# Optimization experiments

Measured on AMD Instinct MI355X. Metric: run time of the kernel, lower is better.

The kernel has to match this reference:

```python
import jax, jax.numpy as jnp
import numpy as np

NUM_HEADS = 16

def setup_inputs() -> dict:
    key = jax.random.key(0)
    ks = jax.random.split(key, 9)
    B, S, H = 2, 2048, 1024
    sc = 0.02
    return {
        "x":  jax.random.normal(ks[0], (B, S, H), jnp.float32),
        "Wq": jax.random.normal(ks[1], (H, H), jnp.float32) * sc,
        "bq": jnp.zeros((H,), jnp.float32),
        "Wk": jax.random.normal(ks[2], (H, H), jnp.float32) * sc,
        "bk": jnp.zeros((H,), jnp.float32),
        "Wv": jax.random.normal(ks[3], (H, H), jnp.float32) * sc,
        "bv": jnp.zeros((H,), jnp.float32),
        "Wo": jax.random.normal(ks[4], (H, H), jnp.float32) * sc,
        "bo": jnp.zeros((H,), jnp.float32),
    }

def _split_heads(t, nh):
    B, S, H = t.shape
    return t.reshape(B, S, nh, H // nh).transpose(0, 2, 1, 3)  # [B, nh, S, hd]

def reference(x, Wq, bq, Wk, bk, Wv, bv, Wo, bo):
    # mask_type == 'gaussian', dropout = 0 (eval), return_weights = False
    B, S, H = x.shape
    nh = NUM_HEADS
    q = _split_heads(x @ Wq + bq, nh)  # [B, nh, S, hd]
    k = _split_heads(x @ Wk + bk, nh)
    v = _split_heads(x @ Wv + bv, nh)
    dif = q - k  # elementwise, as in the original
    # exp(-dif @ dif^T / 2)
    score = jnp.exp(-0.5 * jnp.einsum('bhqd,bhkd->bhqk', dif, dif))
    # gaussian mask: 1 strictly above the diagonal, 0 on/below (faithful to source)
    mask = jnp.triu(jnp.ones((S, S), x.dtype), k=1)
    prob = score * mask  # [B, nh, S, S]
    ctx = jnp.einsum('bhqk,bhkd->bhqd', prob, v)  # [B, nh, S, hd]
    ctx = ctx.transpose(0, 2, 1, 3).reshape(B, S, H)
    return ctx @ Wo + bo
```

## Files before the change

kernel.cpp:

```cpp
#include <hip/hip_runtime.h>
#include <math.h>

constexpr int SEQ  = 2048;
constexpr int HID  = 1024;
constexpr int MTOT = 4096;
constexpr int BH   = 32;

typedef _Float16 f16;
typedef _Float16 f16x8 __attribute__((ext_vector_type(8)));
typedef float    f32x4 __attribute__((ext_vector_type(4)));

__device__ __forceinline__ void gld16(const f16* g, f16* l) {
    __builtin_amdgcn_global_load_lds(
        (__attribute__((address_space(1))) void*)g,
        (__attribute__((address_space(3))) void*)l, 16, 0, 0);
}

__global__ __launch_bounds__(256) void prep(const float* __restrict__ x,
                                            const float* __restrict__ Wq,
                                            const float* __restrict__ Wk,
                                            const float* __restrict__ Wv,
                                            const float* __restrict__ Wo,
                                            f16* __restrict__ xh,
                                            f16* __restrict__ WqkT,
                                            f16* __restrict__ WvT,
                                            f16* __restrict__ WoT) {
    __shared__ f16 T[64][72];
    const int z = blockIdx.z;
    const int t = threadIdx.x;

    if (z == 3) {
        const int chunk = blockIdx.y * 16 + blockIdx.x;
        const float* src = x + (size_t)chunk * 16384;
        f16* dst = xh + (size_t)chunk * 16384;
#pragma unroll
        for (int it = 0; it < 16; it++) {
            const int i = it * 1024 + t * 4;
            float4 v = *(const float4*)(src + i);
            f16 o[4] = {(f16)v.x, (f16)v.y, (f16)v.z, (f16)v.w};
            *(ushort4*)(dst + i) = *(ushort4*)o;
        }
        return;
    }

    const float* W  = (z == 0) ? Wq : (z == 1) ? Wv : Wo;
    f16* WT = (z == 0) ? WqkT : (z == 1) ? WvT : WoT;
    const int k0 = blockIdx.x * 64, n0 = blockIdx.y * 64;
    const int r  = t >> 4;
    const int c4 = (t & 15) * 4;
#pragma unroll
    for (int rr = 0; rr < 64; rr += 16) {
        float4 w = *(const float4*)(W + (size_t)(k0 + rr + r) * HID + n0 + c4);
        if (z == 0) {
            float4 w2 = *(const float4*)(Wk + (size_t)(k0 + rr + r) * HID + n0 + c4);
            w.x -= w2.x; w.y -= w2.y; w.z -= w2.z; w.w -= w2.w;
        }
        T[c4 + 0][rr + r] = (f16)w.x;
        T[c4 + 1][rr + r] = (f16)w.y;
        T[c4 + 2][rr + r] = (f16)w.z;
        T[c4 + 3][rr + r] = (f16)w.w;
    }
    __syncthreads();
#pragma unroll
    for (int pp = 0; pp < 2; pp++) {
        const int nr = pp * 32 + (t >> 3);
        const int kc = (t & 7) * 8;
        *(uint4*)(WT + (size_t)(n0 + nr) * HID + k0 + kc) = *(uint4*)(&T[nr][kc]);
    }
}

__global__ __launch_bounds__(256, 4) void proj_gemm(const f16* __restrict__ A,
                                                    const f16* __restrict__ WqkT,
                                                    const f16* __restrict__ WvT,
                                                    const float* __restrict__ bq,
                                                    const float* __restrict__ bk,
                                                    const float* __restrict__ bv,
                                                    f16* __restrict__ dif,
                                                    f16* __restrict__ vT) {
    __shared__ f16 As[128 * 72];
    __shared__ f16 Bs[64 * 64];
    const int t = threadIdx.x;
    const int m0  = blockIdx.x * 128;
    const int n0g = blockIdx.y * 64;
    const bool isv = (n0g >= HID);
    const f16* BT = isv ? WvT : WqkT;
    const int n0 = n0g & (HID - 1);
    const int w = t >> 6, l = t & 63, quad = l >> 4, ln = l & 15;
    const int wm = w * 32;
    const int xk = ln & 7;

    const int srow8 = l >> 3;
    const int soct  = (l & 7) ^ srow8;
    const f16* pa = A  + (size_t)(m0 + w * 32 + srow8) * HID + soct * 8;
    const f16* pb = BT + (size_t)(n0 + w * 16 + srow8) * HID + soct * 8;

    f32x4 acc[2][4] = {};

    for (int k0 = 0; k0 < HID; k0 += 64) {
        __syncthreads();
#pragma unroll
        for (int c = 0; c < 4; c++)
            gld16(pa + (size_t)c * 8 * HID + k0, As + (w * 4 + c) * 512);
#pragma unroll
        for (int c = 0; c < 2; c++)
            gld16(pb + (size_t)c * 8 * HID + k0, Bs + (w * 2 + c) * 512);
        __syncthreads();

#pragma unroll
        for (int kh = 0; kh < 2; kh++) {
            f16x8 af[2], bf[4];
#pragma unroll
            for (int mt = 0; mt < 2; mt++) {
                const int row = wm + mt * 16 + ln;
                const int oct = (kh * 4 + quad) ^ xk;
                af[mt] = *(const f16x8*)(As + row * 64 + oct * 8);
            }
#pragma unroll
            for (int nt = 0; nt < 4; nt++) {
                const int row = nt * 16 + ln;
                const int oct = (kh * 4 + quad) ^ xk;
                bf[nt] = *(const f16x8*)(Bs + row * 64 + oct * 8);
            }
#pragma unroll
            for (int mt = 0; mt < 2; mt++)
#pragma unroll
                for (int nt = 0; nt < 4; nt++)
                    acc[mt][nt] = __builtin_amdgcn_mfma_f32_16x16x32_f16(
                        af[mt], bf[nt], acc[mt][nt], 0, 0, 0);
        }
    }

    __syncthreads();
    const int b_  = m0 >> 11;
    const int s0g = m0 & 2047;
    const int h_  = n0 >> 6;

    if (!isv) {
        float bb[4];
#pragma unroll
        for (int nt = 0; nt < 4; nt++) {
            const int nl = n0 + nt * 16 + ln;
            bb[nt] = bq[nl] - bk[nl];
        }
#pragma unroll
        for (int mt = 0; mt < 2; mt++)
#pragma unroll
            for (int nt = 0; nt < 4; nt++)
#pragma unroll
                for (int r = 0; r < 4; r++) {
                    const int sl = wm + mt * 16 + quad * 4 + r;
                    As[sl * 72 + nt * 16 + ln] = (f16)(acc[mt][nt][r] + bb[nt]);
                }
        __syncthreads();
        f16* base = dif + ((size_t)(b_ * 16 + h_) * SEQ + s0g) * 64;
        const int sl = t >> 1, eo = (t & 1) * 32;
#pragma unroll
        for (int i = 0; i < 4; i++)
            *(uint4*)(base + (size_t)sl * 64 + eo + i * 8) =
                *(uint4*)(&As[sl * 72 + eo + i * 8]);
    } else {
        float bb[4];
#pragma unroll
        for (int nt = 0; nt < 4; nt++)
            bb[nt] = bv[n0 + nt * 16 + ln];
#pragma unroll
        for (int mt = 0; mt < 2; mt++)
#pragma unroll
            for (int nt = 0; nt < 4; nt++)
#pragma unroll
                for (int r = 0; r < 4; r++) {
                    const int sl = wm + mt * 16 + quad * 4 + r;
                    As[(nt * 16 + ln) * 136 + sl] = (f16)(acc[mt][nt][r] + bb[nt]);
                }
        __syncthreads();
        const int eb = t >> 2, so = (t & 3) * 32;
        f16* base = vT + ((size_t)(b_ * 16 + h_) * 64 + eb) * SEQ + s0g + so;
#pragma unroll
        for (int i = 0; i < 4; i++)
            *(uint4*)(base + i * 8) = *(uint4*)(&As[eb * 136 + so + i * 8]);
    }
}

__global__ __launch_bounds__(256) void out_gemm(const f16* __restrict__ C0,
                                                const f16* __restrict__ C1,
                                                const f16* __restrict__ WoT,
                                                const float* __restrict__ bo,
                                                float* __restrict__ out) {
    __shared__ f16 As[2][128 * 72];
    __shared__ f16 Bs[2][64 * 72];
    const int t = threadIdx.x;
    const int m0 = blockIdx.x * 128, n0 = blockIdx.y * 64;
    const int w = t >> 6, l = t & 63, quad = l >> 4, ln = l & 15;
    const int wm = (w >> 1) * 64, wn = (w & 1) * 32;
    const int arow = t >> 1, ahalf = (t & 1) * 32;
    const int brow = t >> 2, boff = (t & 3) * 16;

    const f16* pa0 = C0  + (size_t)(m0 + arow) * HID + ahalf;
    const f16* pa1 = C1  + (size_t)(m0 + arow) * HID + ahalf;
    const f16* pb  = WoT + (size_t)(n0 + brow) * HID + boff;

    f16x8 a0 = *(const f16x8*)(pa0)      + *(const f16x8*)(pa1);
    f16x8 a1 = *(const f16x8*)(pa0 + 8)  + *(const f16x8*)(pa1 + 8);
    f16x8 a2 = *(const f16x8*)(pa0 + 16) + *(const f16x8*)(pa1 + 16);
    f16x8 a3 = *(const f16x8*)(pa0 + 24) + *(const f16x8*)(pa1 + 24);
    uint4 b0 = *(const uint4*)(pb), b1 = *(const uint4*)(pb + 8);

    f32x4 acc[4][2] = {};
    int buf = 0;

    for (int k0 = 0; k0 < HID; k0 += 64) {
        f16* da = As[buf] + arow * 72 + ahalf;
        *(f16x8*)(da)      = a0; *(f16x8*)(da + 8)  = a1;
        *(f16x8*)(da + 16) = a2; *(f16x8*)(da + 24) = a3;
        f16* db = Bs[buf] + brow * 72 + boff;
        *(uint4*)(db) = b0; *(uint4*)(db + 8) = b1;
        __syncthreads();
        if (k0 + 64 < HID) {
            const int kn = k0 + 64;
            a0 = *(const f16x8*)(pa0 + kn)      + *(const f16x8*)(pa1 + kn);
            a1 = *(const f16x8*)(pa0 + kn + 8)  + *(const f16x8*)(pa1 + kn + 8);
            a2 = *(const f16x8*)(pa0 + kn + 16) + *(const f16x8*)(pa1 + kn + 16);
            a3 = *(const f16x8*)(pa0 + kn + 24) + *(const f16x8*)(pa1 + kn + 24);
            b0 = *(const uint4*)(pb + kn); b1 = *(const uint4*)(pb + kn + 8);
        }
#pragma unroll
        for (int kh = 0; kh < 2; kh++) {
            f16x8 af[4], bf[2];
#pragma unroll
            for (int mt = 0; mt < 4; mt++)
                af[mt] = *(const f16x8*)(As[buf] + (wm + mt * 16 + ln) * 72 + kh * 32 + quad * 8);
#pragma unroll
            for (int nt = 0; nt < 2; nt++)
                bf[nt] = *(const f16x8*)(Bs[buf] + (wn + nt * 16 + ln) * 72 + kh * 32 + quad * 8);
#pragma unroll
            for (int mt = 0; mt < 4; mt++)
#pragma unroll
                for (int nt = 0; nt < 2; nt++)
                    acc[mt][nt] = __builtin_amdgcn_mfma_f32_16x16x32_f16(
                        af[mt], bf[nt], acc[mt][nt], 0, 0, 0);
        }
        buf ^= 1;
    }

#pragma unroll
    for (int mt = 0; mt < 4; mt++)
#pragma unroll
        for (int nt = 0; nt < 2; nt++) {
            const int n = n0 + wn + nt * 16 + ln;
            const float bb = bo[n];
            const int m_base = m0 + wm + mt * 16 + quad * 4;
#pragma unroll
            for (int r = 0; r < 4; r++)
                out[(size_t)(m_base + r) * HID + n] =
                    acc[mt][nt][r] * 65536.0f + bb;
        }
}

__global__ __launch_bounds__(256) void attn_f16(const f16* __restrict__ dif,
                                                const f16* __restrict__ vT,
                                                f16* __restrict__ ctx0,
                                                f16* __restrict__ ctx1) {
    __shared__ f16 Qs[64 * 72];
    __shared__ f16 Ks[64 * 72];
    __shared__ f16 Vs[64 * 72];
    __shared__ f16 Ps[64 * 72];

    const int pq = blockIdx.x, bh = blockIdx.y, ks = blockIdx.z;
    f16* Cout = ks ? ctx1 : ctx0;
    const f16* D  = dif + (size_t)bh * SEQ * 64;
    const f16* VT = vT  + (size_t)bh * 64 * SEQ;
    const int b = bh >> 4, h = bh & 15;
    const int t = threadIdx.x, w = t >> 6, l = t & 63, quad = l >> 4, ln = l & 15;
    const int ve = t >> 2, vc = (t & 3) * 16;

    for (int half = 0; half < 2; half++) {
        const int qt = half ? (31 - pq) : pq;
        const int i0 = qt * 64;
        __syncthreads();

#pragma unroll
        for (int rr = 0; rr < 2; rr++) {
            const int o = rr * 2048 + t * 8;
            uint4 v = *(const uint4*)(D + i0 * 64 + o);
            *(uint4*)(Qs + (o >> 6) * 72 + (o & 63)) = v;
        }
        __syncthreads();
        f16x8 aq[2];
#pragma unroll
        for (int kh = 0; kh < 2; kh++)
            aq[kh] = *(const f16x8*)(Qs + (w * 16 + ln) * 72 + kh * 32 + quad * 8);

        f32x4 acc[4] = {};
        const int kt0 = qt + ks;

        uint4 kr0, kr1, vr0, vr1;
        if (kt0 < 32) {
            const int j0 = kt0 * 64;
            kr0 = *(const uint4*)(D + j0 * 64 + t * 8);
            kr1 = *(const uint4*)(D + j0 * 64 + 2048 + t * 8);
            vr0 = *(const uint4*)(VT + (size_t)ve * SEQ + j0 + vc);
            vr1 = *(const uint4*)(VT + (size_t)ve * SEQ + j0 + vc + 8);
        }

        for (int kt = kt0; kt < 32; kt += 2) {
            __syncthreads();

            {
                const int o0 = t * 8, o1 = 2048 + t * 8;
                *(uint4*)(Ks + (o0 >> 6) * 72 + (o0 & 63)) = kr0;
                *(uint4*)(Ks + (o1 >> 6) * 72 + (o1 & 63)) = kr1;
                *(uint4*)(Vs + ve * 72 + vc)     = vr0;
                *(uint4*)(Vs + ve * 72 + vc + 8) = vr1;
            }
            __syncthreads();

            if (kt + 2 < 32) {
                const int j2 = (kt + 2) * 64;
                kr0 = *(const uint4*)(D + j2 * 64 + t * 8);
                kr1 = *(const uint4*)(D + j2 * 64 + 2048 + t * 8);
                vr0 = *(const uint4*)(VT + (size_t)ve * SEQ + j2 + vc);
                vr1 = *(const uint4*)(VT + (size_t)ve * SEQ + j2 + vc + 8);
            }

            f32x4 s[4] = {};
#pragma unroll
            for (int kh = 0; kh < 2; kh++)
#pragma unroll
                for (int nt = 0; nt < 4; nt++) {
                    f16x8 bfr = *(const f16x8*)(Ks + (nt * 16 + ln) * 72 + kh * 32 + quad * 8);
                    s[nt] = __builtin_amdgcn_mfma_f32_16x16x32_f16(aq[kh], bfr, s[nt], 0, 0, 0);
                }

            const bool full = (kt > qt);
#pragma unroll
            for (int nt = 0; nt < 4; nt++)
#pragma unroll
                for (int r = 0; r < 4; r++) {
                    const int iloc = w * 16 + quad * 4 + r;
                    const int jloc = nt * 16 + ln;
                    float p = (full || (jloc > iloc))
                                  ? fminf(__expf(fmaf(s[nt][r], -0.5f,
                                                      -11.090354888959125f)), 60000.0f)
                                  : 0.0f;
                    Ps[iloc * 72 + jloc] = (f16)p;
                }

#pragma unroll
            for (int kh = 0; kh < 2; kh++) {
                f16x8 a = *(const f16x8*)(Ps + (w * 16 + ln) * 72 + kh * 32 + quad * 8);
#pragma unroll
                for (int nt = 0; nt < 4; nt++) {
                    f16x8 bfr = *(const f16x8*)(Vs + (nt * 16 + ln) * 72 + kh * 32 + quad * 8);
                    acc[nt] = __builtin_amdgcn_mfma_f32_16x16x32_f16(a, bfr, acc[nt], 0, 0, 0);
                }
            }
        }

#pragma unroll
        for (int nt = 0; nt < 4; nt++)
#pragma unroll
            for (int r = 0; r < 4; r++) {
                const int iloc = w * 16 + quad * 4 + r;
                Cout[(size_t)(b * SEQ + i0 + iloc) * HID + h * 64 + nt * 16 + ln] =
                    (f16)acc[nt][r];
            }
    }
}

extern "C" void kernel_launch(void* const* d_in, const int* in_sizes, int n_in,
                              void* d_out, int out_size, void* d_ws, size_t ws_size,
                              hipStream_t stream) {
    const float* x  = (const float*)d_in[0];
    const float* Wq = (const float*)d_in[1];
    const float* bq = (const float*)d_in[2];
    const float* Wk = (const float*)d_in[3];
    const float* bk = (const float*)d_in[4];
    const float* Wv = (const float*)d_in[5];
    const float* bv = (const float*)d_in[6];
    const float* Wo = (const float*)d_in[7];
    const float* bo = (const float*)d_in[8];
    float* out = (float*)d_out;

    char* ws = (char*)d_ws;
    f16* xh   = (f16*)(ws);
    f16* WqkT = (f16*)(ws + (8 << 20));
    f16* WvT  = (f16*)(ws + (10 << 20));
    f16* WoT  = (f16*)(ws + (12 << 20));
    f16* dif  = (f16*)(ws + (14 << 20));
    f16* vT   = (f16*)(ws + (22 << 20));
    f16* ctx0 = (f16*)(ws + (30 << 20));
    f16* ctx1 = (f16*)(ws + (38 << 20));

    prep<<<dim3(16, 16, 4), 256, 0, stream>>>(x, Wq, Wk, Wv, Wo,
                                              xh, WqkT, WvT, WoT);
    proj_gemm<<<dim3(MTOT / 128, 32), 256, 0, stream>>>(xh, WqkT, WvT,
                                                        bq, bk, bv, dif, vT);
    attn_f16<<<dim3(16, BH, 2), 256, 0, stream>>>(dif, vT, ctx0, ctx1);
    out_gemm<<<dim3(MTOT / 128, 16), 256, 0, stream>>>(ctx0, ctx1, WoT, bo, out);
}
```

Baseline: 186.7 us.

## Retile attention warps into 2x2 query/key split with register fragment reuse

Each warp now computes a 32x32 tile of the score matrix instead of a 16-row stripe across all 64 keys. It reuses the Q and K fragments across two MFMAs each, and writes P to shared memory with packed 8-byte stores. The PV product splits along the key dimension, so the two key-half warps' partial context sums are reduced through shared memory at the end. This is meant to cut LDS reads per MFMA. In exchange it adds an extra reduction step with two barriers, holds more accumulator registers, and sets a min-blocks hint of 4 that may constrain register allocation.

```diff
diff --git a/kernel.cpp b/kernel.cpp
--- a/kernel.cpp
+++ b/kernel.cpp
@@ -256,10 +256,10 @@
         }
 }
 
-__global__ __launch_bounds__(256) void attn_f16(const f16* __restrict__ dif,
-                                                const f16* __restrict__ vT,
-                                                f16* __restrict__ ctx0,
-                                                f16* __restrict__ ctx1) {
+__global__ __launch_bounds__(256, 4) void attn_f16(const f16* __restrict__ dif,
+                                                   const f16* __restrict__ vT,
+                                                   f16* __restrict__ ctx0,
+                                                   f16* __restrict__ ctx1) {
     __shared__ f16 Qs[64 * 72];
     __shared__ f16 Ks[64 * 72];
     __shared__ f16 Vs[64 * 72];
@@ -271,6 +271,7 @@
     const f16* VT = vT  + (size_t)bh * 64 * SEQ;
     const int b = bh >> 4, h = bh & 15;
     const int t = threadIdx.x, w = t >> 6, l = t & 63, quad = l >> 4, ln = l & 15;
+    const int qh = w >> 1, jh = w & 1;
     const int ve = t >> 2, vc = (t & 3) * 16;
 
     for (int half = 0; half < 2; half++) {
@@ -285,12 +286,15 @@
             *(uint4*)(Qs + (o >> 6) * 72 + (o & 63)) = v;
         }
         __syncthreads();
-        f16x8 aq[2];
-#pragma unroll
-        for (int kh = 0; kh < 2; kh++)
-            aq[kh] = *(const f16x8*)(Qs + (w * 16 + ln) * 72 + kh * 32 + quad * 8);
-
-        f32x4 acc[4] = {};
+        f16x8 aq[2][2];
+#pragma unroll
+        for (int mt = 0; mt < 2; mt++)
+#pragma unroll
+            for (int kh = 0; kh < 2; kh++)
+                aq[mt][kh] = *(const f16x8*)(Qs + (qh * 32 + mt * 16 + ln) * 72
+                                             + kh * 32 + quad * 8);
+
+        f32x4 acc[2][4] = {};
         const int kt0 = qt + ks;
 
         uint4 kr0, kr1, vr0, vr1;
@@ -303,6 +307,7 @@
         }
 
         for (int kt = kt0; kt < 32; kt += 2) {
+            const int j0 = kt * 64;
             __syncthreads();
 
             {
@@ -322,48 +327,84 @@
                 vr1 = *(const uint4*)(VT + (size_t)ve * SEQ + j2 + vc + 8);
             }
 
-            f32x4 s[4] = {};
+            f32x4 st[2][2] = {};
 #pragma unroll
             for (int kh = 0; kh < 2; kh++)
 #pragma unroll
-                for (int nt = 0; nt < 4; nt++) {
-                    f16x8 bfr = *(const f16x8*)(Ks + (nt * 16 + ln) * 72 + kh * 32 + quad * 8);
-                    s[nt] = __builtin_amdgcn_mfma_f32_16x16x32_f16(aq[kh], bfr, s[nt], 0, 0, 0);
+                for (int nt = 0; nt < 2; nt++) {
+                    f16x8 ak = *(const f16x8*)(Ks + (jh * 32 + nt * 16 + ln) * 72
+                                               + kh * 32 + quad * 8);
+#pragma unroll
+                    for (int mt = 0; mt < 2; mt++)
+                        st[nt][mt] = __builtin_amdgcn_mfma_f32_16x16x32_f16(
+                            ak, aq[mt][kh], st[nt][mt], 0, 0, 0);
                 }
 
             const bool full = (kt > qt);
 #pragma unroll
-            for (int nt = 0; nt < 4; nt++)
-#pragma unroll
-                for (int r = 0; r < 4; r++) {
-                    const int iloc = w * 16 + quad * 4 + r;
-                    const int jloc = nt * 16 + ln;
-                    float p = (full || (jloc > iloc))
-                                  ? fminf(__expf(fmaf(s[nt][r], -0.5f,
-                                                      -11.090354888959125f)), 60000.0f)
-                                  : 0.0f;
-                    Ps[iloc * 72 + jloc] = (f16)p;
+            for (int nt = 0; nt < 2; nt++)
+#pragma unroll
+                for (int mt = 0; mt < 2; mt++) {
+                    const int gi = i0 + qh * 32 + mt * 16 + ln;
+                    f16 pv4[4];
+#pragma unroll
+                    for (int r = 0; r < 4; r++) {
+                        const int gj = j0 + jh * 32 + nt * 16 + quad * 4 + r;
+                        float p = (full || (gj > gi))
+                                      ? fminf(__expf(fmaf(st[nt][mt][r], -0.5f,
+                                                          -11.090354888959125f)),
+                                              60000.0f)
+                                      : 0.0f;
+                        pv4[r] = (f16)p;
+                    }
+                    *(double*)(Ps + (qh * 32 + mt * 16 + ln) * 72
+                               + jh * 32 + nt * 16 + quad * 4) = *(double*)pv4;
                 }
 
-#pragma unroll
-            for (int kh = 0; kh < 2; kh++) {
-                f16x8 a = *(const f16x8*)(Ps + (w * 16 + ln) * 72 + kh * 32 + quad * 8);
-#pragma unroll
-                for (int nt = 0; nt < 4; nt++) {
-                    f16x8 bfr = *(const f16x8*)(Vs + (nt * 16 + ln) * 72 + kh * 32 + quad * 8);
-                    acc[nt] = __builtin_amdgcn_mfma_f32_16x16x32_f16(a, bfr, acc[nt], 0, 0, 0);
+            {
+                f16x8 bv[4];
+#pragma unroll
+                for (int nt = 0; nt < 4; nt++)
+                    bv[nt] = *(const f16x8*)(Vs + (nt * 16 + ln) * 72
+                                             + jh * 32 + quad * 8);
+#pragma unroll
+                for (int mt = 0; mt < 2; mt++) {
+                    f16x8 ap = *(const f16x8*)(Ps + (qh * 32 + mt * 16 + ln) * 72
+                                               + jh * 32 + quad * 8);
+#pragma unroll
+                    for (int nt = 0; nt < 4; nt++)
+                        acc[mt][nt] = __builtin_amdgcn_mfma_f32_16x16x32_f16(
+                            ap, bv[nt], acc[mt][nt], 0, 0, 0);
                 }
             }
         }
 
-#pragma unroll
-        for (int nt = 0; nt < 4; nt++)
-#pragma unroll
-            for (int r = 0; r < 4; r++) {
-                const int iloc = w * 16 + quad * 4 + r;
-                Cout[(size_t)(b * SEQ + i0 + iloc) * HID + h * 64 + nt * 16 + ln] =
-                    (f16)acc[nt][r];
-            }
+        __syncthreads();
+        if (jh == 1) {
+#pragma unroll
+            for (int mt = 0; mt < 2; mt++)
+#pragma unroll
+                for (int nt = 0; nt < 4; nt++)
+#pragma unroll
+                    for (int r = 0; r < 4; r++)
+                        Ps[(qh * 32 + mt * 16 + quad * 4 + r) * 72 + nt * 16 + ln] =
+                            (f16)acc[mt][nt][r];
+        }
+        __syncthreads();
+        if (jh == 0) {
+#pragma unroll
+            for (int mt = 0; mt < 2; mt++)
+#pragma unroll
+                for (int nt = 0; nt < 4; nt++)
+#pragma unroll
+                    for (int r = 0; r < 4; r++) {
+                        const int iloc = qh * 32 + mt * 16 + quad * 4 + r;
+                        float v = acc[mt][nt][r]
+                                + (float)Ps[iloc * 72 + nt * 16 + ln];
+                        Cout[(size_t)(b * SEQ + i0 + iloc) * HID + h * 64
+                             + nt * 16 + ln] = (f16)v;
+                    }
+        }
     }
 }
 
```

Result: no change. 188.0 us (+0.7%).
